# Kernel tuning notes

Hardware: AMD Instinct MI355X
Metric: run time of the kernel (lower is better)

The kernel has to match this reference:

```python
import jax, jax.numpy as jnp
import numpy as np

N_NODES = 50000
N_EDGES = 600000
D_IN = 128
D_HID = 128
D_OUT = 40
EPS = 1e-5


def setup_inputs() -> dict:
    key = jax.random.key(0)
    ks = jax.random.split(key, 16)
    inp = {
        "x": jax.random.normal(ks[0], (N_NODES, D_IN), dtype=jnp.float32),
        "edge_index": jax.random.randint(ks[1], (2, N_EDGES), 0, N_NODES, dtype=jnp.int64),
    }
    dims = [(D_IN, D_HID), (D_HID, D_HID), (D_HID, D_OUT)]
    for i, (di, do) in enumerate(dims):
        s = 1.0 / np.sqrt(di)
        inp[f"W_l{i}"] = jax.random.uniform(ks[2 + 3 * i], (di, do), jnp.float32, -s, s)
        inp[f"b_l{i}"] = jax.random.uniform(ks[3 + 3 * i], (do,), jnp.float32, -s, s)
        inp[f"W_r{i}"] = jax.random.uniform(ks[4 + 3 * i], (di, do), jnp.float32, -s, s)
    for i in range(2):  # num_convs - 1 Trans (LayerNorm) blocks
        inp[f"g{i}"] = jnp.ones((D_HID,), jnp.float32)
        inp[f"be{i}"] = jnp.zeros((D_HID,), jnp.float32)
    return inp


def _sage_conv(x, src, dst, W_l, b_l, W_r):
    # mean-aggregate neighbor features at dst, then lin_l(agg) + lin_r(x)
    msg = jax.ops.segment_sum(x[src], dst, num_segments=N_NODES)  # [N, d]
    deg = jax.ops.segment_sum(jnp.ones((src.shape[0],), x.dtype), dst, num_segments=N_NODES)
    agg = msg / jnp.clip(deg, 1.0)[:, None]
    return agg @ W_l + b_l + x @ W_r


def _trans(x, g, b):
    # LayerNorm -> GELU (exact); Dropout p=0 is identity
    mu = jnp.mean(x, axis=-1, keepdims=True)
    var = jnp.mean(jnp.square(x - mu), axis=-1, keepdims=True)
    xn = (x - mu) * jax.lax.rsqrt(var + EPS) * g + b
    return jax.nn.gelu(xn, approximate=False)


def reference(x, edge_index, W_l0, b_l0, W_r0, W_l1, b_l1, W_r1, W_l2, b_l2, W_r2, g0, be0, g1, be1):
    src, dst = edge_index[0], edge_index[1]
    h = _sage_conv(x, src, dst, W_l0, b_l0, W_r0)
    h = _sage_conv(_trans(h, g0, be0), src, dst, W_l1, b_l1, W_r1)
    h = _sage_conv(_trans(h, g1, be1), src, dst, W_l2, b_l2, W_r2)
    return jax.nn.log_softmax(h, axis=1)
```

## Files before the change

### kernel.cpp

```cpp
#include <hip/hip_runtime.h>
#include <math.h>

#define N_NODES 50000
#define N_EDGES 600000
#define DF 128
#define KK 256
#define DOUT 40
#define EPSN 1e-5f
#define NB1 196

typedef __attribute__((ext_vector_type(8))) short sh8;
typedef __attribute__((ext_vector_type(4))) float f32x4;

__device__ __forceinline__ unsigned short f2b(float f) {
  unsigned u = __builtin_bit_cast(unsigned, f);
  unsigned r = u + 0x7FFFu + ((u >> 16) & 1u);
  return (unsigned short)(r >> 16);
}
__device__ __forceinline__ float b2f(unsigned short b) {
  unsigned u = ((unsigned)b) << 16;
  return __builtin_bit_cast(float, u);
}

__global__ __launch_bounds__(256) void k_count(
    const int* __restrict__ ei, int* __restrict__ counts) {
  int e = blockIdx.x * 256 + threadIdx.x;
  if (e < N_EDGES) atomicAdd(&counts[ei[N_EDGES + e]], 1);
}

__global__ __launch_bounds__(256) void k_bsum(
    const int* __restrict__ counts, int* __restrict__ bsum) {
  int i = blockIdx.x * 256 + threadIdx.x;
  int v = (i < N_NODES) ? counts[i] : 0;
  #pragma unroll
  for (int m = 1; m < 64; m <<= 1) v += __shfl_xor(v, m);
  __shared__ int ws[4];
  if ((threadIdx.x & 63) == 0) ws[threadIdx.x >> 6] = v;
  __syncthreads();
  if (threadIdx.x == 0) bsum[blockIdx.x] = ws[0] + ws[1] + ws[2] + ws[3];
}

__global__ __launch_bounds__(256) void k_bscan(
    const int* __restrict__ bsum, int* __restrict__ bbase) {
  const int t = threadIdx.x, lane = t & 63, w = t >> 6;
  int v = (t < NB1) ? bsum[t] : 0;
  int s = v;
  #pragma unroll
  for (int off = 1; off < 64; off <<= 1) {
    int u = __shfl_up(s, off);
    if (lane >= off) s += u;
  }
  __shared__ int wtot[4];
  if (lane == 63) wtot[w] = s;
  __syncthreads();
  int add = 0;
  for (int k = 0; k < w; ++k) add += wtot[k];
  if (t < NB1) bbase[t] = s + add - v;
}

__global__ __launch_bounds__(256) void k_rowptr(
    const int* __restrict__ counts, const int* __restrict__ bbase,
    int* __restrict__ rowptr, int* __restrict__ cursor,
    float* __restrict__ invdeg) {
  const int i = blockIdx.x * 256 + threadIdx.x;
  const int lane = threadIdx.x & 63, w = threadIdx.x >> 6;
  int c = (i < N_NODES) ? counts[i] : 0;
  int s = c;
  #pragma unroll
  for (int off = 1; off < 64; off <<= 1) {
    int u = __shfl_up(s, off);
    if (lane >= off) s += u;
  }
  __shared__ int wtot[4];
  if (lane == 63) wtot[w] = s;
  __syncthreads();
  int add = bbase[blockIdx.x];
  for (int k = 0; k < w; ++k) add += wtot[k];
  if (i < N_NODES) {
    int excl = s - c + add;
    rowptr[i] = excl;
    cursor[i] = excl;
    invdeg[i] = 1.0f / (float)((c > 1) ? c : 1);
  }
  if (i == 0) rowptr[N_NODES] = N_EDGES;
}

__global__ __launch_bounds__(256) void k_fill(
    const int* __restrict__ ei, int* __restrict__ cursor, int* __restrict__ csr) {
  int e = blockIdx.x * 256 + threadIdx.x;
  if (e < N_EDGES) {
    int d = ei[N_EDGES + e];
    int p = atomicAdd(&cursor[d], 1);
    csr[p] = ei[e];
  }
}

__global__ __launch_bounds__(256) void k_cvt_x(
    const float* __restrict__ x, unsigned* __restrict__ A) {
  int i = blockIdx.x * 256 + threadIdx.x;
  if (i >= N_NODES * 64) return;
  int n = i >> 6, p = i & 63;
  float2 v = ((const float2*)x)[i];
  A[(size_t)n * 128 + 64 + p] = (unsigned)f2b(v.x) | ((unsigned)f2b(v.y) << 16);
}

__global__ __launch_bounds__(256) void k_cvt_w(
    const float* __restrict__ Wl, const float* __restrict__ Wr,
    unsigned short* __restrict__ WT, int Nact, int total) {
  int i = blockIdx.x * 256 + threadIdx.x;
  if (i >= total) return;
  int n = i >> 8, k = i & 255;
  float v = 0.0f;
  if (n < Nact) v = (k < DF) ? Wl[k * Nact + n] : Wr[(k - DF) * Nact + n];
  WT[i] = f2b(v);
}

__global__ __launch_bounds__(256) void k_agg(
    unsigned* __restrict__ A, const int* __restrict__ rowptr,
    const int* __restrict__ csr, const float* __restrict__ invdeg) {
  const int node = (blockIdx.x * 256 + threadIdx.x) >> 6;
  const int lane = threadIdx.x & 63;
  if (node >= N_NODES) return;
  const int beg = rowptr[node], end = rowptr[node + 1];
  float ax = 0.f, ay = 0.f, bx = 0.f, by = 0.f;
  float cx = 0.f, cy = 0.f, dx = 0.f, dy = 0.f;
  int j = beg;
  for (; j + 4 <= end; j += 4) {
    int c0 = csr[j], c1 = csr[j + 1], c2 = csr[j + 2], c3 = csr[j + 3];
    unsigned p0 = A[(size_t)c0 * 128 + 64 + lane];
    unsigned p1 = A[(size_t)c1 * 128 + 64 + lane];
    unsigned p2 = A[(size_t)c2 * 128 + 64 + lane];
    unsigned p3 = A[(size_t)c3 * 128 + 64 + lane];
    ax += b2f((unsigned short)p0); ay += b2f((unsigned short)(p0 >> 16));
    bx += b2f((unsigned short)p1); by += b2f((unsigned short)(p1 >> 16));
    cx += b2f((unsigned short)p2); cy += b2f((unsigned short)(p2 >> 16));
    dx += b2f((unsigned short)p3); dy += b2f((unsigned short)(p3 >> 16));
  }
  for (; j < end; ++j) {
    unsigned p = A[(size_t)csr[j] * 128 + 64 + lane];
    ax += b2f((unsigned short)p); ay += b2f((unsigned short)(p >> 16));
  }
  ax += bx + cx + dx;
  ay += by + cy + dy;
  const float rd = invdeg[node];
  A[(size_t)node * 128 + lane] =
      (unsigned)f2b(ax * rd) | ((unsigned)f2b(ay * rd) << 16);
}

__global__ __launch_bounds__(256) void k_gemm128(
    const unsigned short* __restrict__ Acat, const unsigned short* __restrict__ WT,
    const float* __restrict__ bl, const float* __restrict__ g,
    const float* __restrict__ be, unsigned short* __restrict__ Adst) {
  __shared__ __align__(16) char lds[34816];
  unsigned short* olds = (unsigned short*)lds;
  float2* pp = (float2*)(lds + 32768);

  const int t = threadIdx.x;
  const int rw = blockIdx.x * 64;
  const int wave = t >> 6, lane = t & 63;
  const int lr = lane & 15, lg = lane >> 4;

  #pragma unroll
  for (int it = 0; it < 8; ++it) {
    int id = it * 256 + t;
    int r = id >> 5, c = id & 31;
    int gr = rw + r; if (gr >= N_NODES) gr = N_NODES - 1;
    sh8 v = *(const sh8*)(Acat + (size_t)gr * KK + c * 8);
    unsigned off = (unsigned)((r * 512 + c * 16) ^ ((r & 7) << 4));
    *(sh8*)(lds + off) = v;
  }

  sh8 Bfrag[2][8];
  #pragma unroll
  for (int fl = 0; fl < 2; ++fl) {
    const int n = wave * 32 + fl * 16 + lr;
    const sh8* Bp = (const sh8*)(WT + (size_t)n * KK + lg * 8);
    #pragma unroll
    for (int ks = 0; ks < 8; ++ks) Bfrag[fl][ks] = Bp[ks * 4];
  }
  const int col0 = wave * 32 + lr, col1 = col0 + 16;
  const float bc0 = bl[col0], bc1 = bl[col1];
  const float gv0 = g[col0], gv1 = g[col1];
  const float bev0 = be[col0], bev1 = be[col1];

  __syncthreads();

  f32x4 accs[4][2];
  #pragma unroll
  for (int rf = 0; rf < 4; ++rf)
    #pragma unroll
    for (int fl = 0; fl < 2; ++fl) accs[rf][fl] = (f32x4){0.f, 0.f, 0.f, 0.f};

  #pragma unroll
  for (int ks = 0; ks < 8; ++ks) {
    #pragma unroll
    for (int rf = 0; rf < 4; ++rf) {
      const int r = rf * 16 + lr;
      unsigned off = (unsigned)((r * 512 + ks * 64 + lg * 16) ^ ((r & 7) << 4));
      sh8 a = *(const sh8*)(lds + off);
      accs[rf][0] = __builtin_amdgcn_mfma_f32_16x16x32_bf16(a, Bfrag[0][ks], accs[rf][0], 0, 0, 0);
      accs[rf][1] = __builtin_amdgcn_mfma_f32_16x16x32_bf16(a, Bfrag[1][ks], accs[rf][1], 0, 0, 0);
    }
  }

  #pragma unroll
  for (int rf = 0; rf < 4; ++rf) {
    float sv[4], qv[4];
    #pragma unroll
    for (int r = 0; r < 4; ++r) {
      float v0 = accs[rf][0][r] + bc0;
      float v1 = accs[rf][1][r] + bc1;
      accs[rf][0][r] = v0; accs[rf][1][r] = v1;
      sv[r] = v0 + v1; qv[r] = v0 * v0 + v1 * v1;
    }
    #pragma unroll
    for (int m = 1; m < 16; m <<= 1) {
      #pragma unroll
      for (int r = 0; r < 4; ++r) {
        sv[r] += __shfl_xor(sv[r], m);
        qv[r] += __shfl_xor(qv[r], m);
      }
    }
    if (lr == 0) {
      #pragma unroll
      for (int r = 0; r < 4; ++r)
        pp[wave * 64 + rf * 16 + lg * 4 + r] = make_float2(sv[r], qv[r]);
    }
  }
  __syncthreads();

  #pragma unroll
  for (int rf = 0; rf < 4; ++rf) {
    #pragma unroll
    for (int r = 0; r < 4; ++r) {
      const int row = rf * 16 + lg * 4 + r;
      float2 q0 = pp[row], q1 = pp[64 + row], q2 = pp[128 + row], q3 = pp[192 + row];
      float mu = (q0.x + q1.x + q2.x + q3.x) * (1.0f / 128.0f);
      float var = (q0.y + q1.y + q2.y + q3.y) * (1.0f / 128.0f) - mu * mu;
      float rs = rsqrtf(var + EPSN);
      float xn0 = (accs[rf][0][r] - mu) * rs * gv0 + bev0;
      float xn1 = (accs[rf][1][r] - mu) * rs * gv1 + bev1;
      olds[row * 136 + col0] = f2b(0.5f * xn0 * (1.0f + erff(xn0 * 0.70710678118654752f)));
      olds[row * 136 + col1] = f2b(0.5f * xn1 * (1.0f + erff(xn1 * 0.70710678118654752f)));
    }
  }
  __syncthreads();

  #pragma unroll
  for (int it = 0; it < 4; ++it) {
    int id = it * 256 + t;
    int r = id >> 4, c = id & 15;
    int gr = rw + r;
    if (gr < N_NODES) {
      sh8 v = *(const sh8*)((char*)olds + r * 272 + c * 16);
      *(sh8*)(Adst + (size_t)gr * KK + 128 + c * 8) = v;
    }
  }
}

__global__ __launch_bounds__(256) void k_gemm40(
    const unsigned short* __restrict__ Acat, const unsigned short* __restrict__ WT,
    const float* __restrict__ bl, float* __restrict__ out) {
  __shared__ __align__(16) char lds[43008];
  float* folds = (float*)(lds + 32768);

  const int t = threadIdx.x;
  const int rw = blockIdx.x * 64;
  const int wave = t >> 6, lane = t & 63;
  const int lr = lane & 15, lg = lane >> 4;

  #pragma unroll
  for (int it = 0; it < 8; ++it) {
    int id = it * 256 + t;
    int r = id >> 5, c = id & 31;
    int gr = rw + r; if (gr >= N_NODES) gr = N_NODES - 1;
    sh8 v = *(const sh8*)(Acat + (size_t)gr * KK + c * 8);
    unsigned off = (unsigned)((r * 512 + c * 16) ^ ((r & 7) << 4));
    *(sh8*)(lds + off) = v;
  }

  sh8 Bfrag[3][8];
  #pragma unroll
  for (int f = 0; f < 3; ++f) {
    const int n = f * 16 + lr;
    const sh8* Bp = (const sh8*)(WT + (size_t)n * KK + lg * 8);
    #pragma unroll
    for (int ks = 0; ks < 8; ++ks) Bfrag[f][ks] = Bp[ks * 4];
  }

  __syncthreads();

  f32x4 accs[3];
  #pragma unroll
  for (int f = 0; f < 3; ++f) accs[f] = (f32x4){0.f, 0.f, 0.f, 0.f};

  #pragma unroll
  for (int ks = 0; ks < 8; ++ks) {
    const int r = wave * 16 + lr;
    unsigned off = (unsigned)((r * 512 + ks * 64 + lg * 16) ^ ((r & 7) << 4));
    sh8 a = *(const sh8*)(lds + off);
    #pragma unroll
    for (int f = 0; f < 3; ++f)
      accs[f] = __builtin_amdgcn_mfma_f32_16x16x32_bf16(a, Bfrag[f][ks], accs[f], 0, 0, 0);
  }

  const bool v2 = (lr < 8);
  float vals[3][4];
  #pragma unroll
  for (int f = 0; f < 3; ++f) {
    int col = lr + 16 * f;
    float bc = (col < DOUT) ? bl[col] : 0.0f;
    #pragma unroll
    for (int r = 0; r < 4; ++r) vals[f][r] = accs[f][r] + bc;
  }
  #pragma unroll
  for (int r = 0; r < 4; ++r) {
    float m = fmaxf(vals[0][r], vals[1][r]);
    if (v2) m = fmaxf(m, vals[2][r]);
    #pragma unroll
    for (int k = 1; k < 16; k <<= 1) m = fmaxf(m, __shfl_xor(m, k));
    float se = expf(vals[0][r] - m) + expf(vals[1][r] - m) +
               (v2 ? expf(vals[2][r] - m) : 0.0f);
    #pragma unroll
    for (int k = 1; k < 16; k <<= 1) se += __shfl_xor(se, k);
    float lse = m + logf(se);
    const int row = wave * 16 + lg * 4 + r;
    folds[row * 40 + lr]      = vals[0][r] - lse;
    folds[row * 40 + 16 + lr] = vals[1][r] - lse;
    if (v2) folds[row * 40 + 32 + lr] = vals[2][r] - lse;
  }
  __syncthreads();

  #pragma unroll
  for (int it = 0; it < 3; ++it) {
    int id = it * 256 + t;
    if (id < 640) {
      int r = (id * 6554) >> 16;
      int c = id - r * 10;
      int gr = rw + r;
      if (gr < N_NODES)
        *(float4*)(out + (size_t)gr * DOUT + c * 4) =
            *(const float4*)(folds + r * 40 + c * 4);
    }
  }
}

extern "C" void kernel_launch(void* const* d_in, const int* in_sizes, int n_in,
                              void* d_out, int out_size, void* d_ws, size_t ws_size,
                              hipStream_t stream) {
  const float* x   = (const float*)d_in[0];
  const int*   ei  = (const int*)d_in[1];
  const float* Wl0 = (const float*)d_in[2];
  const float* bl0 = (const float*)d_in[3];
  const float* Wr0 = (const float*)d_in[4];
  const float* Wl1 = (const float*)d_in[5];
  const float* bl1 = (const float*)d_in[6];
  const float* Wr1 = (const float*)d_in[7];
  const float* Wl2 = (const float*)d_in[8];
  const float* bl2 = (const float*)d_in[9];
  const float* Wr2 = (const float*)d_in[10];
  const float* g0  = (const float*)d_in[11];
  const float* be0 = (const float*)d_in[12];
  const float* g1  = (const float*)d_in[13];
  const float* be1 = (const float*)d_in[14];
  float* out = (float*)d_out;

  unsigned short* A   = (unsigned short*)d_ws;
  unsigned short* WT0 = A + (size_t)N_NODES * KK;
  unsigned short* WT1 = WT0 + 128 * KK;
  unsigned short* WT2 = WT1 + 128 * KK;
  float* invdeg = (float*)(WT2 + 48 * KK);
  int*   counts = (int*)(invdeg + N_NODES);
  int*   rowptr = counts + N_NODES;
  int*   cursor = rowptr + N_NODES + 1;
  int*   csr    = cursor + N_NODES;
  int*   bsum   = csr + N_EDGES;
  int*   bbase  = bsum + NB1;

  const int egrid = (N_EDGES + 255) / 256;
  const int xgrid = (N_NODES * 64) / 256;
  const int agrid = (N_NODES * 64) / 256;
  const int ggrid = (N_NODES + 63) / 64;

  hipMemsetAsync(counts, 0, N_NODES * sizeof(int), stream);
  k_count<<<egrid, 256, 0, stream>>>(ei, counts);
  k_bsum<<<NB1, 256, 0, stream>>>(counts, bsum);
  k_bscan<<<1, 256, 0, stream>>>(bsum, bbase);
  k_rowptr<<<NB1, 256, 0, stream>>>(counts, bbase, rowptr, cursor, invdeg);
  k_fill<<<egrid, 256, 0, stream>>>(ei, cursor, csr);

  k_cvt_x<<<xgrid, 256, 0, stream>>>(x, (unsigned*)A);
  k_cvt_w<<<128, 256, 0, stream>>>(Wl0, Wr0, WT0, 128, 128 * KK);
  k_cvt_w<<<128, 256, 0, stream>>>(Wl1, Wr1, WT1, 128, 128 * KK);
  k_cvt_w<<<48, 256, 0, stream>>>(Wl2, Wr2, WT2, DOUT, 48 * KK);

  k_agg<<<agrid, 256, 0, stream>>>((unsigned*)A, rowptr, csr, invdeg);
  k_gemm128<<<ggrid, 256, 0, stream>>>(A, WT0, bl0, g0, be0, A);

  k_agg<<<agrid, 256, 0, stream>>>((unsigned*)A, rowptr, csr, invdeg);
  k_gemm128<<<ggrid, 256, 0, stream>>>(A, WT1, bl1, g1, be1, A);

  k_agg<<<agrid, 256, 0, stream>>>((unsigned*)A, rowptr, csr, invdeg);
  k_gemm40<<<ggrid, 256, 0, stream>>>(A, WT2, bl2, out);
}
```

Before: 253.2 us.

## Fuse neighbor aggregation into SAGE GEMM kernels with ping-pong feature buffers

Moves the mean-aggregation gather into the GEMM kernels, so each block gathers its 64 rows' neighbor sums straight into swizzled LDS and concatenates them with self features, instead of writing aggregated rows to global memory and reloading them. Features now live in two compact N×128 bf16 ping-pong buffers rather than an interleaved N×256 buffer. The three weight-conversion launches are also merged into one. The cost is that each block's aggregation is a serial loop of 16 rows per wave with less parallelism than the standalone aggregation kernel, which may lengthen GEMM blocks and reduce latency hiding.

Result: slower. 426.0 us (+68.3%).

```diff
diff --git a/kernel.cpp b/kernel.cpp
--- a/kernel.cpp
+++ b/kernel.cpp
@@ -96,61 +96,38 @@
 }
 
 __global__ __launch_bounds__(256) void k_cvt_x(
-    const float* __restrict__ x, unsigned* __restrict__ A) {
+    const float* __restrict__ x, unsigned* __restrict__ H) {
   int i = blockIdx.x * 256 + threadIdx.x;
   if (i >= N_NODES * 64) return;
-  int n = i >> 6, p = i & 63;
   float2 v = ((const float2*)x)[i];
-  A[(size_t)n * 128 + 64 + p] = (unsigned)f2b(v.x) | ((unsigned)f2b(v.y) << 16);
-}
-
-__global__ __launch_bounds__(256) void k_cvt_w(
-    const float* __restrict__ Wl, const float* __restrict__ Wr,
-    unsigned short* __restrict__ WT, int Nact, int total) {
+  H[i] = (unsigned)f2b(v.x) | ((unsigned)f2b(v.y) << 16);
+}
+
+__global__ __launch_bounds__(256) void k_cvt_w3(
+    const float* __restrict__ Wl0, const float* __restrict__ Wr0,
+    const float* __restrict__ Wl1, const float* __restrict__ Wr1,
+    const float* __restrict__ Wl2, const float* __restrict__ Wr2,
+    unsigned short* __restrict__ WT0, unsigned short* __restrict__ WT1,
+    unsigned short* __restrict__ WT2) {
   int i = blockIdx.x * 256 + threadIdx.x;
-  if (i >= total) return;
-  int n = i >> 8, k = i & 255;
+  if (i >= 77824) return;
+  const float* Wl; const float* Wr; unsigned short* WT;
+  int j, Nact;
+  if (i < 32768)      { j = i;         Wl = Wl0; Wr = Wr0; WT = WT0; Nact = 128; }
+  else if (i < 65536) { j = i - 32768; Wl = Wl1; Wr = Wr1; WT = WT1; Nact = 128; }
+  else                { j = i - 65536; Wl = Wl2; Wr = Wr2; WT = WT2; Nact = DOUT; }
+  int n = j >> 8, k = j & 255;
   float v = 0.0f;
   if (n < Nact) v = (k < DF) ? Wl[k * Nact + n] : Wr[(k - DF) * Nact + n];
-  WT[i] = f2b(v);
-}
-
-__global__ __launch_bounds__(256) void k_agg(
-    unsigned* __restrict__ A, const int* __restrict__ rowptr,
-    const int* __restrict__ csr, const float* __restrict__ invdeg) {
-  const int node = (blockIdx.x * 256 + threadIdx.x) >> 6;
-  const int lane = threadIdx.x & 63;
-  if (node >= N_NODES) return;
-  const int beg = rowptr[node], end = rowptr[node + 1];
-  float ax = 0.f, ay = 0.f, bx = 0.f, by = 0.f;
-  float cx = 0.f, cy = 0.f, dx = 0.f, dy = 0.f;
-  int j = beg;
-  for (; j + 4 <= end; j += 4) {
-    int c0 = csr[j], c1 = csr[j + 1], c2 = csr[j + 2], c3 = csr[j + 3];
-    unsigned p0 = A[(size_t)c0 * 128 + 64 + lane];
-    unsigned p1 = A[(size_t)c1 * 128 + 64 + lane];
-    unsigned p2 = A[(size_t)c2 * 128 + 64 + lane];
-    unsigned p3 = A[(size_t)c3 * 128 + 64 + lane];
-    ax += b2f((unsigned short)p0); ay += b2f((unsigned short)(p0 >> 16));
-    bx += b2f((unsigned short)p1); by += b2f((unsigned short)(p1 >> 16));
-    cx += b2f((unsigned short)p2); cy += b2f((unsigned short)(p2 >> 16));
-    dx += b2f((unsigned short)p3); dy += b2f((unsigned short)(p3 >> 16));
-  }
-  for (; j < end; ++j) {
-    unsigned p = A[(size_t)csr[j] * 128 + 64 + lane];
-    ax += b2f((unsigned short)p); ay += b2f((unsigned short)(p >> 16));
-  }
-  ax += bx + cx + dx;
-  ay += by + cy + dy;
-  const float rd = invdeg[node];
-  A[(size_t)node * 128 + lane] =
-      (unsigned)f2b(ax * rd) | ((unsigned)f2b(ay * rd) << 16);
-}
-
-__global__ __launch_bounds__(256) void k_gemm128(
-    const unsigned short* __restrict__ Acat, const unsigned short* __restrict__ WT,
+  WT[j] = f2b(v);
+}
+
+__global__ __launch_bounds__(256) void k_sage128(
+    const unsigned short* __restrict__ Hsrc, const unsigned short* __restrict__ WT,
     const float* __restrict__ bl, const float* __restrict__ g,
-    const float* __restrict__ be, unsigned short* __restrict__ Adst) {
+    const float* __restrict__ be,
+    const int* __restrict__ rowptr, const int* __restrict__ csr,
+    const float* __restrict__ invdeg, unsigned short* __restrict__ Hdst) {
   __shared__ __align__(16) char lds[34816];
   unsigned short* olds = (unsigned short*)lds;
   float2* pp = (float2*)(lds + 32768);
@@ -159,16 +136,7 @@
   const int rw = blockIdx.x * 64;
   const int wave = t >> 6, lane = t & 63;
   const int lr = lane & 15, lg = lane >> 4;
-
-  #pragma unroll
-  for (int it = 0; it < 8; ++it) {
-    int id = it * 256 + t;
-    int r = id >> 5, c = id & 31;
-    int gr = rw + r; if (gr >= N_NODES) gr = N_NODES - 1;
-    sh8 v = *(const sh8*)(Acat + (size_t)gr * KK + c * 8);
-    unsigned off = (unsigned)((r * 512 + c * 16) ^ ((r & 7) << 4));
-    *(sh8*)(lds + off) = v;
-  }
+  const unsigned* Hu = (const unsigned*)Hsrc;
 
   sh8 Bfrag[2][8];
   #pragma unroll
@@ -183,6 +151,38 @@
   const float gv0 = g[col0], gv1 = g[col1];
   const float bev0 = be[col0], bev1 = be[col1];
 
+  for (int i = 0; i < 16; ++i) {
+    const int r = wave * 16 + i;
+    int node = rw + r;
+    if (node >= N_NODES) node = N_NODES - 1;
+    const int beg = rowptr[node], end = rowptr[node + 1];
+    float ax = 0.f, ay = 0.f, bx = 0.f, by = 0.f;
+    float cx = 0.f, cy = 0.f, dx = 0.f, dy = 0.f;
+    int j = beg;
+    for (; j + 4 <= end; j += 4) {
+      int c0 = csr[j], c1 = csr[j + 1], c2 = csr[j + 2], c3 = csr[j + 3];
+      unsigned p0 = Hu[(size_t)c0 * 64 + lane];
+      unsigned p1 = Hu[(size_t)c1 * 64 + lane];
+      unsigned p2 = Hu[(size_t)c2 * 64 + lane];
+      unsigned p3 = Hu[(size_t)c3 * 64 + lane];
+      ax += b2f((unsigned short)p0); ay += b2f((unsigned short)(p0 >> 16));
+      bx += b2f((unsigned short)p1); by += b2f((unsigned short)(p1 >> 16));
+      cx += b2f((unsigned short)p2); cy += b2f((unsigned short)(p2 >> 16));
+      dx += b2f((unsigned short)p3); dy += b2f((unsigned short)(p3 >> 16));
+    }
+    for (; j < end; ++j) {
+      unsigned p = Hu[(size_t)csr[j] * 64 + lane];
+      ax += b2f((unsigned short)p); ay += b2f((unsigned short)(p >> 16));
+    }
+    ax += bx + cx + dx;
+    ay += by + cy + dy;
+    const float rd = invdeg[node];
+    unsigned mpack = (unsigned)f2b(ax * rd) | ((unsigned)f2b(ay * rd) << 16);
+    unsigned xpack = Hu[(size_t)node * 64 + lane];
+    const unsigned swz = (unsigned)((r & 7) << 4);
+    *(unsigned*)(lds + ((unsigned)(r * 512 + lane * 4) ^ swz)) = mpack;
+    *(unsigned*)(lds + ((unsigned)(r * 512 + 256 + lane * 4) ^ swz)) = xpack;
+  }
   __syncthreads();
 
   f32x4 accs[4][2];
@@ -253,14 +253,16 @@
     int gr = rw + r;
     if (gr < N_NODES) {
       sh8 v = *(const sh8*)((char*)olds + r * 272 + c * 16);
-      *(sh8*)(Adst + (size_t)gr * KK + 128 + c * 8) = v;
-    }
-  }
-}
-
-__global__ __launch_bounds__(256) void k_gemm40(
-    const unsigned short* __restrict__ Acat, const unsigned short* __restrict__ WT,
-    const float* __restrict__ bl, float* __restrict__ out) {
+      *(sh8*)(Hdst + (size_t)gr * DF + c * 8) = v;
+    }
+  }
+}
+
+__global__ __launch_bounds__(256) void k_sage40(
+    const unsigned short* __restrict__ Hsrc, const unsigned short* __restrict__ WT,
+    const float* __restrict__ bl,
+    const int* __restrict__ rowptr, const int* __restrict__ csr,
+    const float* __restrict__ invdeg, float* __restrict__ out) {
   __shared__ __align__(16) char lds[43008];
   float* folds = (float*)(lds + 32768);
 
@@ -268,16 +270,7 @@
   const int rw = blockIdx.x * 64;
   const int wave = t >> 6, lane = t & 63;
   const int lr = lane & 15, lg = lane >> 4;
-
-  #pragma unroll
-  for (int it = 0; it < 8; ++it) {
-    int id = it * 256 + t;
-    int r = id >> 5, c = id & 31;
-    int gr = rw + r; if (gr >= N_NODES) gr = N_NODES - 1;
-    sh8 v = *(const sh8*)(Acat + (size_t)gr * KK + c * 8);
-    unsigned off = (unsigned)((r * 512 + c * 16) ^ ((r & 7) << 4));
-    *(sh8*)(lds + off) = v;
-  }
+  const unsigned* Hu = (const unsigned*)Hsrc;
 
   sh8 Bfrag[3][8];
   #pragma unroll
@@ -288,6 +281,38 @@
     for (int ks = 0; ks < 8; ++ks) Bfrag[f][ks] = Bp[ks * 4];
   }
 
+  for (int i = 0; i < 16; ++i) {
+    const int r = wave * 16 + i;
+    int node = rw + r;
+    if (node >= N_NODES) node = N_NODES - 1;
+    const int beg = rowptr[node], end = rowptr[node + 1];
+    float ax = 0.f, ay = 0.f, bx = 0.f, by = 0.f;
+    float cx = 0.f, cy = 0.f, dx = 0.f, dy = 0.f;
+    int j = beg;
+    for (; j + 4 <= end; j += 4) {
+      int c0 = csr[j], c1 = csr[j + 1], c2 = csr[j + 2], c3 = csr[j + 3];
+      unsigned p0 = Hu[(size_t)c0 * 64 + lane];
+      unsigned p1 = Hu[(size_t)c1 * 64 + lane];
+      unsigned p2 = Hu[(size_t)c2 * 64 + lane];
+      unsigned p3 = Hu[(size_t)c3 * 64 + lane];
+      ax += b2f((unsigned short)p0); ay += b2f((unsigned short)(p0 >> 16));
+      bx += b2f((unsigned short)p1); by += b2f((unsigned short)(p1 >> 16));
+      cx += b2f((unsigned short)p2); cy += b2f((unsigned short)(p2 >> 16));
+      dx += b2f((unsigned short)p3); dy += b2f((unsigned short)(p3 >> 16));
+    }
+    for (; j < end; ++j) {
+      unsigned p = Hu[(size_t)csr[j] * 64 + lane];
+      ax += b2f((unsigned short)p); ay += b2f((unsigned short)(p >> 16));
+    }
+    ax += bx + cx + dx;
+    ay += by + cy + dy;
+    const float rd = invdeg[node];
+    unsigned mpack = (unsigned)f2b(ax * rd) | ((unsigned)f2b(ay * rd) << 16);
+    unsigned xpack = Hu[(size_t)node * 64 + lane];
+    const unsigned swz = (unsigned)((r & 7) << 4);
+    *(unsigned*)(lds + ((unsigned)(r * 512 + lane * 4) ^ swz)) = mpack;
+    *(unsigned*)(lds + ((unsigned)(r * 512 + 256 + lane * 4) ^ swz)) = xpack;
+  }
   __syncthreads();
 
   f32x4 accs[3];
@@ -365,8 +390,9 @@
   const float* be1 = (const float*)d_in[14];
   float* out = (float*)d_out;
 
-  unsigned short* A   = (unsigned short*)d_ws;
-  unsigned short* WT0 = A + (size_t)N_NODES * KK;
+  unsigned short* H0  = (unsigned short*)d_ws;
+  unsigned short* H1  = H0 + (size_t)N_NODES * DF;
+  unsigned short* WT0 = H1 + (size_t)N_NODES * DF;
   unsigned short* WT1 = WT0 + 128 * KK;
   unsigned short* WT2 = WT1 + 128 * KK;
   float* invdeg = (float*)(WT2 + 48 * KK);
@@ -379,8 +405,7 @@
 
   const int egrid = (N_EDGES + 255) / 256;
   const int xgrid = (N_NODES * 64) / 256;
-  const int agrid = (N_NODES * 64) / 256;
-  const int ggrid = (N_NODES + 63) / 64;
+  const int sgrid = (N_NODES + 63) / 64;
 
   hipMemsetAsync(counts, 0, N_NODES * sizeof(int), stream);
   k_count<<<egrid, 256, 0, stream>>>(ei, counts);
@@ -389,17 +414,10 @@
   k_rowptr<<<NB1, 256, 0, stream>>>(counts, bbase, rowptr, cursor, invdeg);
   k_fill<<<egrid, 256, 0, stream>>>(ei, cursor, csr);
 
-  k_cvt_x<<<xgrid, 256, 0, stream>>>(x, (unsigned*)A);
-  k_cvt_w<<<128, 256, 0, stream>>>(Wl0, Wr0, WT0, 128, 128 * KK);
-  k_cvt_w<<<128, 256, 0, stream>>>(Wl1, Wr1, WT1, 128, 128 * KK);
-  k_cvt_w<<<48, 256, 0, stream>>>(Wl2, Wr2, WT2, DOUT, 48 * KK);
-
-  k_agg<<<agrid, 256, 0, stream>>>((unsigned*)A, rowptr, csr, invdeg);
-  k_gemm128<<<ggrid, 256, 0, stream>>>(A, WT0, bl0, g0, be0, A);
-
-  k_agg<<<agrid, 256, 0, stream>>>((unsigned*)A, rowptr, csr, invdeg);
-  k_gemm128<<<ggrid, 256, 0, stream>>>(A, WT1, bl1, g1, be1, A);
-
-  k_agg<<<agrid, 256, 0, stream>>>((unsigned*)A, rowptr, csr, invdeg);
-  k_gemm40<<<ggrid, 256, 0, stream>>>(A, WT2, bl2, out);
-}
+  k_cvt_x<<<xgrid, 256, 0, stream>>>(x, (unsigned*)H0);
+  k_cvt_w3<<<304, 256, 0, stream>>>(Wl0, Wr0, Wl1, Wr1, Wl2, Wr2, WT0, WT1, WT2);
+
+  k_sage128<<<sgrid, 256, 0, stream>>>(H0, WT0, bl0, g0, be0, rowptr, csr, invdeg, H1);
+  k_sage128<<<sgrid, 256, 0, stream>>>(H1, WT1, bl1, g1, be1, rowptr, csr, invdeg, H0);
+  k_sage40<<<sgrid, 256, 0, stream>>>(H0, WT2, bl2, rowptr, csr, invdeg, out);
+}
```

## Reorder last layer to project-then-aggregate and shrink gemm128 tiles

Applied to the files above, without the earlier changes.

The last SAGE layer first projects node features through W_l2 and W_r2 into an 80-wide bf16 buffer. It then aggregates the 40-wide projected neighbor rows and fuses bias and log_softmax in a new kernel. This avoids gathering 128-wide features for the final aggregation, at the cost of an extra bf16 rounding on the projected values before summation. It also cuts gemm128 tiles to 16 rows per block to raise block count and lower LDS use, and merges the three weight-conversion launches into one.

Result: faster. 242.7 us (-4.2%).

```diff
diff --git a/kernel.cpp b/kernel.cpp
--- a/kernel.cpp
+++ b/kernel.cpp
@@ -20,6 +20,9 @@
 __device__ __forceinline__ float b2f(unsigned short b) {
   unsigned u = ((unsigned)b) << 16;
   return __builtin_bit_cast(float, u);
+}
+__device__ __forceinline__ float gelu_f(float x) {
+  return 0.5f * x * (1.0f + erff(x * 0.70710678118654752f));
 }
 
 __global__ __launch_bounds__(256) void k_count(
@@ -104,15 +107,27 @@
   A[(size_t)n * 128 + 64 + p] = (unsigned)f2b(v.x) | ((unsigned)f2b(v.y) << 16);
 }
 
-__global__ __launch_bounds__(256) void k_cvt_w(
-    const float* __restrict__ Wl, const float* __restrict__ Wr,
-    unsigned short* __restrict__ WT, int Nact, int total) {
+__global__ __launch_bounds__(256) void k_cvt_w3(
+    const float* __restrict__ Wl0, const float* __restrict__ Wr0,
+    const float* __restrict__ Wl1, const float* __restrict__ Wr1,
+    const float* __restrict__ Wl2, const float* __restrict__ Wr2,
+    unsigned short* __restrict__ WT0, unsigned short* __restrict__ WT1,
+    unsigned short* __restrict__ WT2b) {
   int i = blockIdx.x * 256 + threadIdx.x;
-  if (i >= total) return;
-  int n = i >> 8, k = i & 255;
-  float v = 0.0f;
-  if (n < Nact) v = (k < DF) ? Wl[k * Nact + n] : Wr[(k - DF) * Nact + n];
-  WT[i] = f2b(v);
+  if (i >= 75776) return;
+  if (i < 65536) {
+    const float* Wl; const float* Wr; unsigned short* WT; int j;
+    if (i < 32768) { j = i;         Wl = Wl0; Wr = Wr0; WT = WT0; }
+    else           { j = i - 32768; Wl = Wl1; Wr = Wr1; WT = WT1; }
+    int n = j >> 8, k = j & 255;
+    float v = (k < DF) ? Wl[k * DF + n] : Wr[(k - DF) * DF + n];
+    WT[j] = f2b(v);
+  } else {
+    int j = i - 65536;
+    int n = j >> 7, k = j & 127;
+    float v = (n < DOUT) ? Wl2[k * DOUT + n] : Wr2[k * DOUT + (n - DOUT)];
+    WT2b[j] = f2b(v);
+  }
 }
 
 __global__ __launch_bounds__(256) void k_agg(
@@ -151,183 +166,143 @@
     const unsigned short* __restrict__ Acat, const unsigned short* __restrict__ WT,
     const float* __restrict__ bl, const float* __restrict__ g,
     const float* __restrict__ be, unsigned short* __restrict__ Adst) {
-  __shared__ __align__(16) char lds[34816];
+  __shared__ __align__(16) char lds[8704];
   unsigned short* olds = (unsigned short*)lds;
-  float2* pp = (float2*)(lds + 32768);
-
+  float2* pp = (float2*)(lds + 8192);
+
+  const int t = threadIdx.x;
+  const int rw = blockIdx.x * 16;
+  const int wave = t >> 6, lane = t & 63;
+  const int lr = lane & 15, lg = lane >> 4;
+
+  #pragma unroll
+  for (int it = 0; it < 2; ++it) {
+    int id = it * 256 + t;
+    int r = id >> 5, c = id & 31;
+    sh8 v = *(const sh8*)(Acat + (size_t)(rw + r) * KK + c * 8);
+    unsigned off = (unsigned)((r * 512 + c * 16) ^ ((r & 7) << 4));
+    *(sh8*)(lds + off) = v;
+  }
+
+  sh8 Bfrag[2][8];
+  #pragma unroll
+  for (int fl = 0; fl < 2; ++fl) {
+    const int n = wave * 32 + fl * 16 + lr;
+    const sh8* Bp = (const sh8*)(WT + (size_t)n * KK + lg * 8);
+    #pragma unroll
+    for (int ks = 0; ks < 8; ++ks) Bfrag[fl][ks] = Bp[ks * 4];
+  }
+  const int col0 = wave * 32 + lr, col1 = col0 + 16;
+  const float bc0 = bl[col0], bc1 = bl[col1];
+  const float gv0 = g[col0], gv1 = g[col1];
+  const float bev0 = be[col0], bev1 = be[col1];
+
+  __syncthreads();
+
+  f32x4 acc0 = {0.f, 0.f, 0.f, 0.f}, acc1 = {0.f, 0.f, 0.f, 0.f};
+  #pragma unroll
+  for (int ks = 0; ks < 8; ++ks) {
+    unsigned off = (unsigned)((lr * 512 + ks * 64 + lg * 16) ^ ((lr & 7) << 4));
+    sh8 a = *(const sh8*)(lds + off);
+    acc0 = __builtin_amdgcn_mfma_f32_16x16x32_bf16(a, Bfrag[0][ks], acc0, 0, 0, 0);
+    acc1 = __builtin_amdgcn_mfma_f32_16x16x32_bf16(a, Bfrag[1][ks], acc1, 0, 0, 0);
+  }
+
+  float sv[4], qv[4];
+  #pragma unroll
+  for (int r = 0; r < 4; ++r) {
+    float v0 = acc0[r] + bc0, v1 = acc1[r] + bc1;
+    acc0[r] = v0; acc1[r] = v1;
+    sv[r] = v0 + v1; qv[r] = v0 * v0 + v1 * v1;
+  }
+  #pragma unroll
+  for (int m = 1; m < 16; m <<= 1) {
+    #pragma unroll
+    for (int r = 0; r < 4; ++r) {
+      sv[r] += __shfl_xor(sv[r], m);
+      qv[r] += __shfl_xor(qv[r], m);
+    }
+  }
+  if (lr == 0) {
+    #pragma unroll
+    for (int r = 0; r < 4; ++r)
+      pp[wave * 16 + lg * 4 + r] = make_float2(sv[r], qv[r]);
+  }
+  __syncthreads();
+
+  #pragma unroll
+  for (int r = 0; r < 4; ++r) {
+    const int row = lg * 4 + r;
+    float2 a0 = pp[row], a1 = pp[16 + row], a2 = pp[32 + row], a3 = pp[48 + row];
+    float mu = (a0.x + a1.x + a2.x + a3.x) * (1.0f / 128.0f);
+    float var = (a0.y + a1.y + a2.y + a3.y) * (1.0f / 128.0f) - mu * mu;
+    float rs = rsqrtf(var + EPSN);
+    float xn0 = (acc0[r] - mu) * rs * gv0 + bev0;
+    float xn1 = (acc1[r] - mu) * rs * gv1 + bev1;
+    olds[row * 136 + col0] = f2b(gelu_f(xn0));
+    olds[row * 136 + col1] = f2b(gelu_f(xn1));
+  }
+  __syncthreads();
+
+  {
+    int r = t >> 4, c = t & 15;
+    sh8 v = *(const sh8*)((char*)olds + r * 272 + c * 16);
+    *(sh8*)(Adst + (size_t)(rw + r) * KK + 128 + c * 8) = v;
+  }
+}
+
+__global__ __launch_bounds__(256) void k_gemm80(
+    const unsigned short* __restrict__ Acat, const unsigned short* __restrict__ WT,
+    unsigned short* __restrict__ PQ) {
+  __shared__ __align__(16) char lds[16384];
   const int t = threadIdx.x;
   const int rw = blockIdx.x * 64;
   const int wave = t >> 6, lane = t & 63;
   const int lr = lane & 15, lg = lane >> 4;
 
   #pragma unroll
-  for (int it = 0; it < 8; ++it) {
-    int id = it * 256 + t;
-    int r = id >> 5, c = id & 31;
-    int gr = rw + r; if (gr >= N_NODES) gr = N_NODES - 1;
-    sh8 v = *(const sh8*)(Acat + (size_t)gr * KK + c * 8);
-    unsigned off = (unsigned)((r * 512 + c * 16) ^ ((r & 7) << 4));
-    *(sh8*)(lds + off) = v;
-  }
-
-  sh8 Bfrag[2][8];
-  #pragma unroll
-  for (int fl = 0; fl < 2; ++fl) {
-    const int n = wave * 32 + fl * 16 + lr;
-    const sh8* Bp = (const sh8*)(WT + (size_t)n * KK + lg * 8);
-    #pragma unroll
-    for (int ks = 0; ks < 8; ++ks) Bfrag[fl][ks] = Bp[ks * 4];
-  }
-  const int col0 = wave * 32 + lr, col1 = col0 + 16;
-  const float bc0 = bl[col0], bc1 = bl[col1];
-  const float gv0 = g[col0], gv1 = g[col1];
-  const float bev0 = be[col0], bev1 = be[col1];
-
-  __syncthreads();
-
-  f32x4 accs[4][2];
-  #pragma unroll
-  for (int rf = 0; rf < 4; ++rf)
-    #pragma unroll
-    for (int fl = 0; fl < 2; ++fl) accs[rf][fl] = (f32x4){0.f, 0.f, 0.f, 0.f};
-
-  #pragma unroll
-  for (int ks = 0; ks < 8; ++ks) {
-    #pragma unroll
-    for (int rf = 0; rf < 4; ++rf) {
-      const int r = rf * 16 + lr;
-      unsigned off = (unsigned)((r * 512 + ks * 64 + lg * 16) ^ ((r & 7) << 4));
-      sh8 a = *(const sh8*)(lds + off);
-      accs[rf][0] = __builtin_amdgcn_mfma_f32_16x16x32_bf16(a, Bfrag[0][ks], accs[rf][0], 0, 0, 0);
-      accs[rf][1] = __builtin_amdgcn_mfma_f32_16x16x32_bf16(a, Bfrag[1][ks], accs[rf][1], 0, 0, 0);
-    }
-  }
-
-  #pragma unroll
-  for (int rf = 0; rf < 4; ++rf) {
-    float sv[4], qv[4];
-    #pragma unroll
-    for (int r = 0; r < 4; ++r) {
-      float v0 = accs[rf][0][r] + bc0;
-      float v1 = accs[rf][1][r] + bc1;
-      accs[rf][0][r] = v0; accs[rf][1][r] = v1;
-      sv[r] = v0 + v1; qv[r] = v0 * v0 + v1 * v1;
-    }
-    #pragma unroll
-    for (int m = 1; m < 16; m <<= 1) {
-      #pragma unroll
-      for (int r = 0; r < 4; ++r) {
-        sv[r] += __shfl_xor(sv[r], m);
-        qv[r] += __shfl_xor(qv[r], m);
-      }
-    }
-    if (lr == 0) {
-      #pragma unroll
-      for (int r = 0; r < 4; ++r)
-        pp[wave * 64 + rf * 16 + lg * 4 + r] = make_float2(sv[r], qv[r]);
-    }
-  }
-  __syncthreads();
-
-  #pragma unroll
-  for (int rf = 0; rf < 4; ++rf) {
-    #pragma unroll
-    for (int r = 0; r < 4; ++r) {
-      const int row = rf * 16 + lg * 4 + r;
-      float2 q0 = pp[row], q1 = pp[64 + row], q2 = pp[128 + row], q3 = pp[192 + row];
-      float mu = (q0.x + q1.x + q2.x + q3.x) * (1.0f / 128.0f);
-      float var = (q0.y + q1.y + q2.y + q3.y) * (1.0f / 128.0f) - mu * mu;
-      float rs = rsqrtf(var + EPSN);
-      float xn0 = (accs[rf][0][r] - mu) * rs * gv0 + bev0;
-      float xn1 = (accs[rf][1][r] - mu) * rs * gv1 + bev1;
-      olds[row * 136 + col0] = f2b(0.5f * xn0 * (1.0f + erff(xn0 * 0.70710678118654752f)));
-      olds[row * 136 + col1] = f2b(0.5f * xn1 * (1.0f + erff(xn1 * 0.70710678118654752f)));
-    }
-  }
-  __syncthreads();
-
-  #pragma unroll
   for (int it = 0; it < 4; ++it) {
     int id = it * 256 + t;
     int r = id >> 4, c = id & 15;
-    int gr = rw + r;
-    if (gr < N_NODES) {
-      sh8 v = *(const sh8*)((char*)olds + r * 272 + c * 16);
-      *(sh8*)(Adst + (size_t)gr * KK + 128 + c * 8) = v;
+    int gr = rw + r; if (gr >= N_NODES) gr = N_NODES - 1;
+    sh8 v = *(const sh8*)(Acat + (size_t)gr * KK + 128 + c * 8);
+    unsigned off = (unsigned)((r * 256 + c * 16) ^ ((r & 7) << 4));
+    *(sh8*)(lds + off) = v;
+  }
+
+  sh8 Bfrag[5][4];
+  #pragma unroll
+  for (int f = 0; f < 5; ++f) {
+    const int n = f * 16 + lr;
+    const sh8* Bp = (const sh8*)(WT + (size_t)n * 128 + lg * 8);
+    #pragma unroll
+    for (int ks = 0; ks < 4; ++ks) Bfrag[f][ks] = Bp[ks * 4];
+  }
+  __syncthreads();
+
+  f32x4 accs[5];
+  #pragma unroll
+  for (int f = 0; f < 5; ++f) accs[f] = (f32x4){0.f, 0.f, 0.f, 0.f};
+
+  #pragma unroll
+  for (int ks = 0; ks < 4; ++ks) {
+    const int r = wave * 16 + lr;
+    unsigned off = (unsigned)((r * 256 + ks * 64 + lg * 16) ^ ((r & 7) << 4));
+    sh8 a = *(const sh8*)(lds + off);
+    #pragma unroll
+    for (int f = 0; f < 5; ++f)
+      accs[f] = __builtin_amdgcn_mfma_f32_16x16x32_bf16(a, Bfrag[f][ks], accs[f], 0, 0, 0);
+  }
+  __syncthreads();
+
+  unsigned short* olds = (unsigned short*)lds;
+  #pragma unroll
+  for (int f = 0; f < 5; ++f) {
+    #pragma unroll
+    for (int r = 0; r < 4; ++r) {
+      const int row = wave * 16 + lg * 4 + r;
+      olds[row * 80 + f * 16 + lr] = f2b(accs[f][r]);
     }
-  }
-}
-
-__global__ __launch_bounds__(256) void k_gemm40(
-    const unsigned short* __restrict__ Acat, const unsigned short* __restrict__ WT,
-    const float* __restrict__ bl, float* __restrict__ out) {
-  __shared__ __align__(16) char lds[43008];
-  float* folds = (float*)(lds + 32768);
-
-  const int t = threadIdx.x;
-  const int rw = blockIdx.x * 64;
-  const int wave = t >> 6, lane = t & 63;
-  const int lr = lane & 15, lg = lane >> 4;
-
-  #pragma unroll
-  for (int it = 0; it < 8; ++it) {
-    int id = it * 256 + t;
-    int r = id >> 5, c = id & 31;
-    int gr = rw + r; if (gr >= N_NODES) gr = N_NODES - 1;
-    sh8 v = *(const sh8*)(Acat + (size_t)gr * KK + c * 8);
-    unsigned off = (unsigned)((r * 512 + c * 16) ^ ((r & 7) << 4));
-    *(sh8*)(lds + off) = v;
-  }
-
-  sh8 Bfrag[3][8];
-  #pragma unroll
-  for (int f = 0; f < 3; ++f) {
-    const int n = f * 16 + lr;
-    const sh8* Bp = (const sh8*)(WT + (size_t)n * KK + lg * 8);
-    #pragma unroll
-    for (int ks = 0; ks < 8; ++ks) Bfrag[f][ks] = Bp[ks * 4];
-  }
-
-  __syncthreads();
-
-  f32x4 accs[3];
-  #pragma unroll
-  for (int f = 0; f < 3; ++f) accs[f] = (f32x4){0.f, 0.f, 0.f, 0.f};
-
-  #pragma unroll
-  for (int ks = 0; ks < 8; ++ks) {
-    const int r = wave * 16 + lr;
-    unsigned off = (unsigned)((r * 512 + ks * 64 + lg * 16) ^ ((r & 7) << 4));
-    sh8 a = *(const sh8*)(lds + off);
-    #pragma unroll
-    for (int f = 0; f < 3; ++f)
-      accs[f] = __builtin_amdgcn_mfma_f32_16x16x32_bf16(a, Bfrag[f][ks], accs[f], 0, 0, 0);
-  }
-
-  const bool v2 = (lr < 8);
-  float vals[3][4];
-  #pragma unroll
-  for (int f = 0; f < 3; ++f) {
-    int col = lr + 16 * f;
-    float bc = (col < DOUT) ? bl[col] : 0.0f;
-    #pragma unroll
-    for (int r = 0; r < 4; ++r) vals[f][r] = accs[f][r] + bc;
-  }
-  #pragma unroll
-  for (int r = 0; r < 4; ++r) {
-    float m = fmaxf(vals[0][r], vals[1][r]);
-    if (v2) m = fmaxf(m, vals[2][r]);
-    #pragma unroll
-    for (int k = 1; k < 16; k <<= 1) m = fmaxf(m, __shfl_xor(m, k));
-    float se = expf(vals[0][r] - m) + expf(vals[1][r] - m) +
-               (v2 ? expf(vals[2][r] - m) : 0.0f);
-    #pragma unroll
-    for (int k = 1; k < 16; k <<= 1) se += __shfl_xor(se, k);
-    float lse = m + logf(se);
-    const int row = wave * 16 + lg * 4 + r;
-    folds[row * 40 + lr]      = vals[0][r] - lse;
-    folds[row * 40 + 16 + lr] = vals[1][r] - lse;
-    if (v2) folds[row * 40 + 32 + lr] = vals[2][r] - lse;
   }
   __syncthreads();
 
@@ -339,10 +314,57 @@
       int c = id - r * 10;
       int gr = rw + r;
       if (gr < N_NODES)
-        *(float4*)(out + (size_t)gr * DOUT + c * 4) =
-            *(const float4*)(folds + r * 40 + c * 4);
+        *(sh8*)(PQ + (size_t)gr * 80 + c * 8) =
+            *(const sh8*)((char*)olds + r * 160 + c * 16);
     }
   }
+}
+
+__global__ __launch_bounds__(256) void k_final(
+    const unsigned short* __restrict__ PQ, const float* __restrict__ bl,
+    const int* __restrict__ rowptr, const int* __restrict__ csr,
+    const float* __restrict__ invdeg, float* __restrict__ out) {
+  const int node = blockIdx.x * 8 + (threadIdx.x >> 5);
+  const int hl = threadIdx.x & 31;
+  const bool act = (hl < 20);
+  const int l = act ? hl : 0;
+  const unsigned* Pu = (const unsigned*)PQ;
+
+  const int beg = rowptr[node], end = rowptr[node + 1];
+  float ax = 0.f, ay = 0.f, bx = 0.f, by = 0.f;
+  float cx = 0.f, cy = 0.f, dx = 0.f, dy = 0.f;
+  int j = beg;
+  for (; j + 4 <= end; j += 4) {
+    int c0 = csr[j], c1 = csr[j + 1], c2 = csr[j + 2], c3 = csr[j + 3];
+    unsigned p0 = Pu[(size_t)c0 * 40 + l];
+    unsigned p1 = Pu[(size_t)c1 * 40 + l];
+    unsigned p2 = Pu[(size_t)c2 * 40 + l];
+    unsigned p3 = Pu[(size_t)c3 * 40 + l];
+    ax += b2f((unsigned short)p0); ay += b2f((unsigned short)(p0 >> 16));
+    bx += b2f((unsigned short)p1); by += b2f((unsigned short)(p1 >> 16));
+    cx += b2f((unsigned short)p2); cy += b2f((unsigned short)(p2 >> 16));
+    dx += b2f((unsigned short)p3); dy += b2f((unsigned short)(p3 >> 16));
+  }
+  for (; j < end; ++j) {
+    unsigned p = Pu[(size_t)csr[j] * 40 + l];
+    ax += b2f((unsigned short)p); ay += b2f((unsigned short)(p >> 16));
+  }
+  ax += bx + cx + dx;
+  ay += by + cy + dy;
+  const float rd = invdeg[node];
+  unsigned q = Pu[(size_t)node * 40 + 20 + l];
+  float v0 = ax * rd + b2f((unsigned short)q) + bl[2 * l];
+  float v1 = ay * rd + b2f((unsigned short)(q >> 16)) + bl[2 * l + 1];
+
+  float m = act ? fmaxf(v0, v1) : -INFINITY;
+  #pragma unroll
+  for (int k = 1; k < 32; k <<= 1) m = fmaxf(m, __shfl_xor(m, k));
+  float se = act ? (expf(v0 - m) + expf(v1 - m)) : 0.0f;
+  #pragma unroll
+  for (int k = 1; k < 32; k <<= 1) se += __shfl_xor(se, k);
+  float lse = m + logf(se);
+  if (act)
+    ((float2*)out)[(size_t)node * 20 + hl] = make_float2(v0 - lse, v1 - lse);
 }
 
 extern "C" void kernel_launch(void* const* d_in, const int* in_sizes, int n_in,
@@ -365,11 +387,12 @@
   const float* be1 = (const float*)d_in[14];
   float* out = (float*)d_out;
 
-  unsigned short* A   = (unsigned short*)d_ws;
-  unsigned short* WT0 = A + (size_t)N_NODES * KK;
-  unsigned short* WT1 = WT0 + 128 * KK;
-  unsigned short* WT2 = WT1 + 128 * KK;
-  float* invdeg = (float*)(WT2 + 48 * KK);
+  unsigned short* A    = (unsigned short*)d_ws;
+  unsigned short* PQ   = A + (size_t)N_NODES * KK;
+  unsigned short* WT0  = PQ + (size_t)N_NODES * 80;
+  unsigned short* WT1  = WT0 + 128 * KK;
+  unsigned short* WT2b = WT1 + 128 * KK;
+  float* invdeg = (float*)(WT2b + 80 * 128);
   int*   counts = (int*)(invdeg + N_NODES);
   int*   rowptr = counts + N_NODES;
   int*   cursor = rowptr + N_NODES + 1;
@@ -380,7 +403,9 @@
   const int egrid = (N_EDGES + 255) / 256;
   const int xgrid = (N_NODES * 64) / 256;
   const int agrid = (N_NODES * 64) / 256;
-  const int ggrid = (N_NODES + 63) / 64;
+  const int g128  = N_NODES / 16;
+  const int g80   = (N_NODES + 63) / 64;
+  const int fgrid = N_NODES / 8;
 
   hipMemsetAsync(counts, 0, N_NODES * sizeof(int), stream);
   k_count<<<egrid, 256, 0, stream>>>(ei, counts);
@@ -390,16 +415,14 @@
   k_fill<<<egrid, 256, 0, stream>>>(ei, cursor, csr);
 
   k_cvt_x<<<xgrid, 256, 0, stream>>>(x, (unsigned*)A);
-  k_cvt_w<<<128, 256, 0, stream>>>(Wl0, Wr0, WT0, 128, 128 * KK);
-  k_cvt_w<<<128, 256, 0, stream>>>(Wl1, Wr1, WT1, 128, 128 * KK);
-  k_cvt_w<<<48, 256, 0, stream>>>(Wl2, Wr2, WT2, DOUT, 48 * KK);
+  k_cvt_w3<<<296, 256, 0, stream>>>(Wl0, Wr0, Wl1, Wr1, Wl2, Wr2, WT0, WT1, WT2b);
 
   k_agg<<<agrid, 256, 0, stream>>>((unsigned*)A, rowptr, csr, invdeg);
-  k_gemm128<<<ggrid, 256, 0, stream>>>(A, WT0, bl0, g0, be0, A);
+  k_gemm128<<<g128, 256, 0, stream>>>(A, WT0, bl0, g0, be0, A);
 
   k_agg<<<agrid, 256, 0, stream>>>((unsigned*)A, rowptr, csr, invdeg);
-  k_gemm128<<<ggrid, 256, 0, stream>>>(A, WT1, bl1, g1, be1, A);
-
-  k_agg<<<agrid, 256, 0, stream>>>((unsigned*)A, rowptr, csr, invdeg);
-  k_gemm40<<<ggrid, 256, 0, stream>>>(A, WT2, bl2, out);
-}
+  k_gemm128<<<g128, 256, 0, stream>>>(A, WT1, bl1, g1, be1, A);
+
+  k_gemm80<<<g80, 256, 0, stream>>>(A, WT2b, PQ);
+  k_final<<<fgrid, 256, 0, stream>>>(PQ, bl2, rowptr, csr, invdeg, out);
+}
```
